# Performance work log

Hardware: AMD Instinct MI355X
Metric: run time of the kernel (lower is better)

Reference implementation:

```python
import jax, jax.numpy as jnp
import numpy as np
import math

D_MODEL = 512
N_HEADS = 8
MAX_SPAN = 512
SPAN_LOSS_COEF = 2e-4
NEG_INF = -1.0e9
R_SIZE = 4.0


def soft_span_mask(span, max_span, seq_len):
    # span: (H,) clamped span fractions
    i_idx = jnp.arange(seq_len, dtype=span.dtype)[:, None]
    j_idx = jnp.arange(seq_len, dtype=span.dtype)[None, :]
    dist = i_idx - j_idx                                  # (T, T)
    eff_span = (span * max_span)[:, None, None]           # (H, 1, 1)
    x = eff_span - dist[None, :, :]                       # (H, T, T)
    R = jnp.clip((x + 1.0) / R_SIZE, 0.0, 1.0)
    causal_ok = dist[None, :, :] >= 0
    log_R = jnp.maximum(jnp.log(R + 1e-10), NEG_INF)
    return jnp.where(causal_ok & (R > 0), log_R, NEG_INF)  # (H, T, T)


def setup_inputs() -> dict:
    key = jax.random.key(0)
    ks = jax.random.split(key, 6)
    B, T, D = 4, 2048, D_MODEL
    w_scale = 0.02
    return {
        "x": jax.random.normal(ks[0], (B, T, D), dtype=jnp.float32),
        "wq": jax.random.normal(ks[1], (D, D), dtype=jnp.float32) * w_scale,
        "wk": jax.random.normal(ks[2], (D, D), dtype=jnp.float32) * w_scale,
        "wv": jax.random.normal(ks[3], (D, D), dtype=jnp.float32) * w_scale,
        "wo": jax.random.normal(ks[4], (D, D), dtype=jnp.float32) * w_scale,
        "span_params": jax.random.uniform(ks[5], (N_HEADS,), dtype=jnp.float32),
    }


def reference(x, wq, wk, wv, wo, span_params):
    B, T, D = x.shape
    H = N_HEADS
    d_h = D // H

    clamped_span = jnp.clip(span_params, 0.0, 1.0)

    # nn.Linear(bias=False): y = x @ W.T
    Q = (x @ wq.T).reshape(B, T, H, d_h).transpose(0, 2, 1, 3)  # (B,H,T,dh)
    K = (x @ wk.T).reshape(B, T, H, d_h).transpose(0, 2, 1, 3)
    V = (x @ wv.T).reshape(B, T, H, d_h).transpose(0, 2, 1, 3)

    scale = 1.0 / math.sqrt(d_h)
    scores = jnp.einsum("bhqd,bhkd->bhqk", Q, K) * scale        # (B,H,T,T)
    scores = scores + soft_span_mask(clamped_span, MAX_SPAN, T)[None]

    weights = jax.nn.softmax(scores, axis=-1)
    out = jnp.einsum("bhqk,bhkd->bhqd", weights, V)             # (B,H,T,dh)
    out = out.transpose(0, 2, 1, 3).reshape(B, T, D)
    output = out @ wo.T

    span_loss = SPAN_LOSS_COEF * clamped_span.mean()
    return output, span_loss
```

## Files before the change

kernel.cpp:

```cpp
#include <hip/hip_runtime.h>
#include <math.h>

#define T_SEQ   2048
#define DMODEL  512
#define NHEADS  8
#define DH      64
#define NEG_INF -1.0e9f

typedef __attribute__((ext_vector_type(8))) short short8;
typedef __attribute__((ext_vector_type(4))) float f32x4;
typedef unsigned int u32;
typedef unsigned short u16;

__device__ __forceinline__ u16 f2bf(float f) {
    union { float f; u32 u; } w; w.f = f;
    return (u16)((w.u + 0x8000u) >> 16);
}

__device__ __forceinline__ void async_load16(const u16* g, u16* l) {
    __builtin_amdgcn_global_load_lds(
        (const __attribute__((address_space(1))) u32*)(const void*)g,
        (__attribute__((address_space(3))) u32*)(void*)l, 16, 0, 0);
}

__global__ void cast_all(const float* __restrict__ x,  const float* __restrict__ wq,
                         const float* __restrict__ wk, const float* __restrict__ wv,
                         const float* __restrict__ wo, const float* __restrict__ sp,
                         u16* __restrict__ xb,  u16* __restrict__ wqb,
                         u16* __restrict__ wkb, u16* __restrict__ wvb,
                         u16* __restrict__ wob, float* __restrict__ loss_out)
{
    const int bid = blockIdx.x;
    const float* src; u16* dst; int i;
    if (bid < 4096) { src = x; dst = xb; i = bid * 256 + threadIdx.x; }
    else {
        const int wsel = (bid - 4096) >> 8;
        src = (wsel == 0) ? wq : (wsel == 1) ? wk : (wsel == 2) ? wv : wo;
        dst = (wsel == 0) ? wqb : (wsel == 1) ? wkb : (wsel == 2) ? wvb : wob;
        i = ((bid - 4096) & 255) * 256 + threadIdx.x;
    }
    float4 v = ((const float4*)src)[i];
    ushort4 o;
    o.x = f2bf(v.x); o.y = f2bf(v.y); o.z = f2bf(v.z); o.w = f2bf(v.w);
    ((ushort4*)dst)[i] = o;
    if (bid == 5119 && threadIdx.x == 0) {
        float s = 0.0f;
        for (int h = 0; h < NHEADS; ++h)
            s += fminf(fmaxf(sp[h], 0.0f), 1.0f);
        loss_out[0] = 2e-4f * (s * 0.125f);
    }
}

__global__ __launch_bounds__(256)
void gemm_bf16(const u16* __restrict__ A,
               const u16* __restrict__ W0, const u16* __restrict__ W1,
               const u16* __restrict__ W2,
               u16* __restrict__ Cb0, u16* __restrict__ Cb1,
               u16* __restrict__ Cb2,
               float* __restrict__ Cf, int scatter)
{
    constexpr int K = 512, BK = 64;
    const u16* W  = (blockIdx.z == 0) ? W0 : (blockIdx.z == 1) ? W1 : W2;
    u16*       Cb = (blockIdx.z == 0) ? Cb0 : (blockIdx.z == 1) ? Cb1 : Cb2;

    __shared__ __align__(16) u16 smem[16384];
    u16* As = smem;
    u16* Bs = smem + 8192;

    const int t    = threadIdx.x;
    const int lane = t & 63;
    const int wave = t >> 6;
    const int wm   = wave >> 1, wn = wave & 1;
    const int m0   = blockIdx.x * 128, n0 = blockIdx.y * 128;

    const int srow = t >> 3;
    const int kb   = (t & 7) ^ (srow & 7);
    const u16* gA = A + (size_t)(m0 + srow) * K + kb * 8;
    const u16* gW = W + (size_t)(n0 + srow) * K + kb * 8;

    const int rA = wm * 64 + (lane & 15);
    const int rB = wn * 64 + (lane & 15);
    const int kq = lane >> 4;
    const int offA0 = rA * BK + ((kq      ^ (rA & 7)) * 8);
    const int offA1 = rA * BK + (((4 + kq) ^ (rA & 7)) * 8);
    const int offB0 = rB * BK + ((kq      ^ (rB & 7)) * 8);
    const int offB1 = rB * BK + (((4 + kq) ^ (rB & 7)) * 8);

    f32x4 acc[4][4];
#pragma unroll
    for (int it = 0; it < 4; ++it)
#pragma unroll
        for (int jt = 0; jt < 4; ++jt) acc[it][jt] = (f32x4)0.0f;

    for (int k0 = 0; k0 < K; k0 += BK) {
        __syncthreads();
#pragma unroll
        for (int i = 0; i < 4; ++i) {
            async_load16(gA + k0 + i * (32 * K), As + t * 8 + i * 2048);
            async_load16(gW + k0 + i * (32 * K), Bs + t * 8 + i * 2048);
        }
        __syncthreads();

        short8 af[4][2], bfr[4][2];
#pragma unroll
        for (int it = 0; it < 4; ++it) {
            af[it][0]  = *(const short8*)(As + offA0 + it * 16 * BK);
            af[it][1]  = *(const short8*)(As + offA1 + it * 16 * BK);
            bfr[it][0] = *(const short8*)(Bs + offB0 + it * 16 * BK);
            bfr[it][1] = *(const short8*)(Bs + offB1 + it * 16 * BK);
        }
#pragma unroll
        for (int it = 0; it < 4; ++it)
#pragma unroll
            for (int jt = 0; jt < 4; ++jt) {
                acc[it][jt] = __builtin_amdgcn_mfma_f32_16x16x32_bf16(
                    af[it][0], bfr[jt][0], acc[it][jt], 0, 0, 0);
                acc[it][jt] = __builtin_amdgcn_mfma_f32_16x16x32_bf16(
                    af[it][1], bfr[jt][1], acc[it][jt], 0, 0, 0);
            }
    }

    const int r0 = (lane >> 4) * 4;
    const int cl = lane & 15;

    if (scatter) {
        const bool vt_mode = (blockIdx.z == 2);
        constexpr int P = 136;
#pragma unroll
        for (int rnd = 0; rnd < 2; ++rnd) {
            __syncthreads();
#pragma unroll
            for (int s = 0; s < 2; ++s) {
                const int it = rnd * 2 + s;
                const int lrow = wm * 32 + s * 16 + r0;
#pragma unroll
                for (int jt = 0; jt < 4; ++jt) {
                    const int cc = wn * 64 + jt * 16 + cl;
#pragma unroll
                    for (int r = 0; r < 4; ++r)
                        smem[(lrow + r) * P + cc] = f2bf(acc[it][jt][r]);
                }
            }
            __syncthreads();
            if (!vt_mode) {
                const int lrow2 = t >> 2;
                const int h2    = (t >> 1) & 1;
                const int dhalf = t & 1;
                const int grow  = m0 + (lrow2 >> 5) * 64 + rnd * 32 + (lrow2 & 31);
                const int b     = grow >> 11, tt = grow & 2047;
                const int h     = (n0 >> 6) + h2;
                u16* dst = Cb + ((size_t)((b * NHEADS + h) * T_SEQ + tt)) * DH + dhalf * 32;
                const u16* srcl = smem + lrow2 * P + h2 * 64 + dhalf * 32;
#pragma unroll
                for (int i = 0; i < 4; ++i)
                    ((uint4*)dst)[i] = *(const uint4*)(srcl + i * 8);
            } else {
                const int hd   = t >> 1;
                const int run  = t & 1;
                const int h    = (n0 >> 6) + (hd >> 6);
                const int d    = hd & 63;
                const int tb   = m0 + run * 64 + rnd * 32;
                const int b    = tb >> 11;
                u16* dst = Cb + (((size_t)(b * NHEADS + h) * DH + d) << 11) + (tb & 2047);
                union { uint4 v[4]; u16 s[32]; } pk;
#pragma unroll
                for (int i = 0; i < 32; ++i)
                    pk.s[i] = smem[(run * 32 + i) * P + hd];
#pragma unroll
                for (int i = 0; i < 4; ++i)
                    ((uint4*)dst)[i] = pk.v[i];
            }
        }
    } else {
#pragma unroll
        for (int it = 0; it < 4; ++it) {
#pragma unroll
            for (int r = 0; r < 4; ++r) {
                const int row = m0 + wm * 64 + it * 16 + r0 + r;
#pragma unroll
                for (int jt = 0; jt < 4; ++jt) {
                    const int col = n0 + wn * 64 + jt * 16 + cl;
                    Cf[(size_t)row * DMODEL + col] = acc[it][jt][r];
                }
            }
        }
    }
}

__global__ __launch_bounds__(256)
void attn_mfma(const u16* __restrict__ Q, const u16* __restrict__ K,
               const u16* __restrict__ Vt, const float* __restrict__ span_params,
               u16* __restrict__ out)
{
    __shared__ __align__(16) u16 Ks[64 * 64];
    __shared__ __align__(16) u16 Vs[64 * 64];
    __shared__ __align__(16) u16 Ps[4][16 * 76];

    const int tid  = threadIdx.x;
    const int lane = tid & 63;
    const int w    = tid >> 6;
    const int nl   = lane & 15;
    const int quad = lane >> 4;
    const int b    = blockIdx.x & 3;
    const int h    = blockIdx.x >> 2;
    const int bh   = b * NHEADS + h;
    const int i0   = blockIdx.y * 64;
    const int q0   = i0 + w * 16;

    const u16* Qh = Q  + (size_t)bh * (T_SEQ * DH);
    const u16* Kh = K  + (size_t)bh * (T_SEQ * DH);
    const u16* Vh = Vt + (size_t)bh * (DH * T_SEQ);

    float span = span_params[h];
    span = fminf(fmaxf(span, 0.0f), 1.0f);
    const float eff_span = span * 512.0f;
    const int wspan = (int)(eff_span + 1.0f) + 1;

    short8 qf0 = *(const short8*)(Qh + (size_t)(q0 + nl) * DH + quad * 8);
    short8 qf1 = *(const short8*)(Qh + (size_t)(q0 + nl) * DH + 32 + quad * 8);

    const int srow = tid >> 2;
    const int p    = tid & 3;
    const int sw0  = ((2 * p)     ^ (srow & 7)) * 8;
    const int sw1  = ((2 * p + 1) ^ (srow & 7)) * 8;
    const u16* gK = Kh + (size_t)srow * DH + p * 16;
    const u16* gV = Vh + (size_t)srow * T_SEQ + p * 16;
    u16* lK = Ks + srow * 64;
    u16* lV = Vs + srow * 64;

    f32x4 o[4];
    float m_r[4], l_r[4];
#pragma unroll
    for (int d = 0; d < 4; ++d) o[d] = (f32x4)0.0f;
#pragma unroll
    for (int r = 0; r < 4; ++r) { m_r[r] = -1.0e30f; l_r[r] = 0.0f; }

    int j_lo = i0 - wspan;
    if (j_lo < 0) j_lo = 0;
    j_lo &= ~63;

    uint4 kr0 = *(const uint4*)(gK + (size_t)j_lo * DH);
    uint4 kr1 = *(const uint4*)(gK + (size_t)j_lo * DH + 8);
    uint4 vr0 = *(const uint4*)(gV + j_lo);
    uint4 vr1 = *(const uint4*)(gV + j_lo + 8);

    for (int j0 = j_lo; j0 <= i0; j0 += 64) {
        __syncthreads();
        *(uint4*)(lK + sw0) = kr0;
        *(uint4*)(lK + sw1) = kr1;
        *(uint4*)(lV + sw0) = vr0;
        *(uint4*)(lV + sw1) = vr1;
        __syncthreads();

        if (j0 < i0) {
            const int jn = j0 + 64;
            kr0 = *(const uint4*)(gK + (size_t)jn * DH);
            kr1 = *(const uint4*)(gK + (size_t)jn * DH + 8);
            vr0 = *(const uint4*)(gV + jn);
            vr1 = *(const uint4*)(gV + jn + 8);
        }

        f32x4 s[4];
        bool any[4];
#pragma unroll
        for (int n = 0; n < 4; ++n) {
            const int jn = j0 + n * 16;
            any[n] = (jn <= q0 + 15) &&
                     ((float)(q0 - jn - 15) < eff_span + 1.0f);
            s[n] = (f32x4)0.0f;
            if (any[n]) {
                const int row = n * 16 + nl;
                const u16* kp = Ks + row * 64;
                short8 b0 = *(const short8*)(kp + ((quad ^ (row & 7)) * 8));
                short8 b1 = *(const short8*)(kp + (((4 + quad) ^ (row & 7)) * 8));
                s[n] = __builtin_amdgcn_mfma_f32_16x16x32_bf16(qf0, b0, s[n], 0, 0, 0);
                s[n] = __builtin_amdgcn_mfma_f32_16x16x32_bf16(qf1, b1, s[n], 0, 0, 0);
            }
        }

        float tmax[4] = {-1.0e30f, -1.0e30f, -1.0e30f, -1.0e30f};
#pragma unroll
        for (int n = 0; n < 4; ++n) {
            if (!any[n]) continue;
            const int jn = j0 + n * 16;
            const bool causal_b = (jn + 15 > q0);
            const bool span_b   = ((float)(q0 + 15 - jn) > eff_span - 3.0f);
            if (!causal_b && !span_b) {
#pragma unroll
                for (int r = 0; r < 4; ++r) {
                    const float sv = s[n][r] * 0.125f;
                    s[n][r] = sv;
                    tmax[r] = fmaxf(tmax[r], sv);
                }
            } else if (!span_b) {
#pragma unroll
                for (int r = 0; r < 4; ++r) {
                    const int dist = (q0 + quad * 4 + r) - (jn + nl);
                    const float sv = (dist >= 0) ? s[n][r] * 0.125f : NEG_INF;
                    s[n][r] = sv;
                    tmax[r] = fmaxf(tmax[r], sv);
                }
            } else {
#pragma unroll
                for (int r = 0; r < 4; ++r) {
                    const int dist = (q0 + quad * 4 + r) - (jn + nl);
                    float sv = NEG_INF;
                    if (dist >= 0) {
                        float xv = eff_span - (float)dist;
                        float R  = fminf(fmaxf((xv + 1.0f) * 0.25f, 0.0f), 1.0f);
                        if (R > 0.0f)
                            sv = s[n][r] * 0.125f +
                                 ((R < 1.0f) ? __logf(R + 1e-10f) : 0.0f);
                    }
                    s[n][r] = sv;
                    tmax[r] = fmaxf(tmax[r], sv);
                }
            }
        }

        float alpha[4];
#pragma unroll
        for (int r = 0; r < 4; ++r) {
            float t = tmax[r];
            t = fmaxf(t, __shfl_xor(t, 1));
            t = fmaxf(t, __shfl_xor(t, 2));
            t = fmaxf(t, __shfl_xor(t, 4));
            t = fmaxf(t, __shfl_xor(t, 8));
            const float m_new = fmaxf(m_r[r], t);
            alpha[r] = __expf(m_r[r] - m_new);
            m_r[r] = m_new;
        }

        float psum[4] = {0.0f, 0.0f, 0.0f, 0.0f};
#pragma unroll
        for (int n = 0; n < 4; ++n) {
            if (any[n]) {
#pragma unroll
                for (int r = 0; r < 4; ++r) {
                    const float pv = __expf(s[n][r] - m_r[r]);
                    psum[r] += pv;
                    Ps[w][(quad * 4 + r) * 76 + n * 16 + nl] = f2bf(pv);
                }
            } else {
#pragma unroll
                for (int r = 0; r < 4; ++r)
                    Ps[w][(quad * 4 + r) * 76 + n * 16 + nl] = 0;
            }
        }
#pragma unroll
        for (int r = 0; r < 4; ++r) {
            float ps = psum[r];
            ps += __shfl_xor(ps, 1);
            ps += __shfl_xor(ps, 2);
            ps += __shfl_xor(ps, 4);
            ps += __shfl_xor(ps, 8);
            l_r[r] = l_r[r] * alpha[r] + ps;
#pragma unroll
            for (int d = 0; d < 4; ++d) o[d][r] *= alpha[r];
        }

        const bool kf0 = any[0] | any[1];
        const bool kf1 = any[2] | any[3];
        const u16* pb = Ps[w] + nl * 76;
        short8 a0 = *(const short8*)(pb + quad * 8);
        short8 a1 = *(const short8*)(pb + 32 + quad * 8);
#pragma unroll
        for (int d = 0; d < 4; ++d) {
            const int vrow = d * 16 + nl;
            const u16* vp = Vs + vrow * 64;
            if (kf0) {
                short8 vb0 = *(const short8*)(vp + ((quad ^ (vrow & 7)) * 8));
                o[d] = __builtin_amdgcn_mfma_f32_16x16x32_bf16(a0, vb0, o[d], 0, 0, 0);
            }
            if (kf1) {
                short8 vb1 = *(const short8*)(vp + (((4 + quad) ^ (vrow & 7)) * 8));
                o[d] = __builtin_amdgcn_mfma_f32_16x16x32_bf16(a1, vb1, o[d], 0, 0, 0);
            }
        }
    }

#pragma unroll
    for (int r = 0; r < 4; ++r) {
        const int qg = q0 + quad * 4 + r;
        const float inv_l = 1.0f / l_r[r];
        u16* op = out + (size_t)(b * T_SEQ + qg) * DMODEL + h * 64;
#pragma unroll
        for (int d = 0; d < 4; ++d)
            op[d * 16 + nl] = f2bf(o[d][r] * inv_l);
    }
}

extern "C" void kernel_launch(void* const* d_in, const int* in_sizes, int n_in,
                              void* d_out, int out_size, void* d_ws, size_t ws_size,
                              hipStream_t stream)
{
    (void)in_sizes; (void)n_in; (void)out_size; (void)ws_size;
    const float* x  = (const float*)d_in[0];
    const float* wq = (const float*)d_in[1];
    const float* wk = (const float*)d_in[2];
    const float* wv = (const float*)d_in[3];
    const float* wo = (const float*)d_in[4];
    const float* sp = (const float*)d_in[5];
    float* out = (float*)d_out;

    const size_t elems = (size_t)4 * T_SEQ * DMODEL;
    u16* xb  = (u16*)d_ws;
    u16* Qb  = xb  + elems;
    u16* Kb  = Qb  + elems;
    u16* Vtb = Kb  + elems;
    u16* Ab  = Vtb + elems;
    u16* wqb = Ab  + elems;
    u16* wkb = wqb + 262144;
    u16* wvb = wkb + 262144;
    u16* wob = wvb + 262144;

    cast_all<<<5120, 256, 0, stream>>>(x, wq, wk, wv, wo, sp,
                                       xb, wqb, wkb, wvb, wob, out + elems);
    gemm_bf16<<<dim3(64, 4, 3), 256, 0, stream>>>(
        xb, wqb, wkb, wvb, Qb, Kb, Vtb, nullptr, 1);
    attn_mfma<<<dim3(32, 32), 256, 0, stream>>>(Qb, Kb, Vtb, sp, Ab);
    gemm_bf16<<<dim3(64, 4, 1), 256, 0, stream>>>(
        Ab, wob, wob, wob, nullptr, nullptr, nullptr, out, 0);
}
```

Baseline: 171.4 us.

## Use single-wave attention blocks reading K/V from global, register-prefetch GEMM tiles

The attention kernel becomes one wave per 16-query block. It drops the shared K/V staging and block barriers, and each wave reads K and V fragments straight from global memory (relying on cache). This lets each wave iterate only over its own span window and removes synchronisation between waves, at the cost of redundant global/L2 traffic across waves that share keys. The GEMM replaces async global-to-LDS loads with register prefetch of the next K tile and sets a 3-block occupancy hint. The block-index mapping also staggers heads per batch.

```diff
diff --git a/kernel.cpp b/kernel.cpp
--- a/kernel.cpp
+++ b/kernel.cpp
@@ -15,12 +15,6 @@
 __device__ __forceinline__ u16 f2bf(float f) {
     union { float f; u32 u; } w; w.f = f;
     return (u16)((w.u + 0x8000u) >> 16);
-}
-
-__device__ __forceinline__ void async_load16(const u16* g, u16* l) {
-    __builtin_amdgcn_global_load_lds(
-        (const __attribute__((address_space(1))) u32*)(const void*)g,
-        (__attribute__((address_space(3))) u32*)(void*)l, 16, 0, 0);
 }
 
 __global__ void cast_all(const float* __restrict__ x,  const float* __restrict__ wq,
@@ -51,7 +45,7 @@
     }
 }
 
-__global__ __launch_bounds__(256)
+__global__ __launch_bounds__(256, 3)
 void gemm_bf16(const u16* __restrict__ A,
                const u16* __restrict__ W0, const u16* __restrict__ W1,
                const u16* __restrict__ W2,
@@ -92,14 +86,29 @@
 #pragma unroll
         for (int jt = 0; jt < 4; ++jt) acc[it][jt] = (f32x4)0.0f;
 
+    uint4 ar[4], wr[4];
+#pragma unroll
+    for (int i = 0; i < 4; ++i) {
+        ar[i] = *(const uint4*)(gA + i * (32 * K));
+        wr[i] = *(const uint4*)(gW + i * (32 * K));
+    }
+
     for (int k0 = 0; k0 < K; k0 += BK) {
         __syncthreads();
 #pragma unroll
         for (int i = 0; i < 4; ++i) {
-            async_load16(gA + k0 + i * (32 * K), As + t * 8 + i * 2048);
-            async_load16(gW + k0 + i * (32 * K), Bs + t * 8 + i * 2048);
+            *(uint4*)(As + t * 8 + i * 2048) = ar[i];
+            *(uint4*)(Bs + t * 8 + i * 2048) = wr[i];
         }
         __syncthreads();
+
+        if (k0 + BK < K) {
+#pragma unroll
+            for (int i = 0; i < 4; ++i) {
+                ar[i] = *(const uint4*)(gA + (k0 + BK) + i * (32 * K));
+                wr[i] = *(const uint4*)(gW + (k0 + BK) + i * (32 * K));
+            }
+        }
 
         short8 af[4][2], bfr[4][2];
 #pragma unroll
@@ -187,25 +196,21 @@
     }
 }
 
-__global__ __launch_bounds__(256)
-void attn_mfma(const u16* __restrict__ Q, const u16* __restrict__ K,
+__global__ __launch_bounds__(64, 4)
+void attn_wave(const u16* __restrict__ Q, const u16* __restrict__ K,
                const u16* __restrict__ Vt, const float* __restrict__ span_params,
                u16* __restrict__ out)
 {
-    __shared__ __align__(16) u16 Ks[64 * 64];
-    __shared__ __align__(16) u16 Vs[64 * 64];
-    __shared__ __align__(16) u16 Ps[4][16 * 76];
-
-    const int tid  = threadIdx.x;
-    const int lane = tid & 63;
-    const int w    = tid >> 6;
+    __shared__ __align__(16) u16 Ps[16 * 72];
+
+    const int lane = threadIdx.x;
     const int nl   = lane & 15;
     const int quad = lane >> 4;
-    const int b    = blockIdx.x & 3;
-    const int h    = blockIdx.x >> 2;
+    const int xi   = blockIdx.x;
+    const int b    = xi >> 3;
+    const int h    = ((xi & 7) + 5 * b) & 7;
     const int bh   = b * NHEADS + h;
-    const int i0   = blockIdx.y * 64;
-    const int q0   = i0 + w * 16;
+    const int q0   = blockIdx.y * 16;
 
     const u16* Qh = Q  + (size_t)bh * (T_SEQ * DH);
     const u16* Kh = K  + (size_t)bh * (T_SEQ * DH);
@@ -219,15 +224,6 @@
     short8 qf0 = *(const short8*)(Qh + (size_t)(q0 + nl) * DH + quad * 8);
     short8 qf1 = *(const short8*)(Qh + (size_t)(q0 + nl) * DH + 32 + quad * 8);
 
-    const int srow = tid >> 2;
-    const int p    = tid & 3;
-    const int sw0  = ((2 * p)     ^ (srow & 7)) * 8;
-    const int sw1  = ((2 * p + 1) ^ (srow & 7)) * 8;
-    const u16* gK = Kh + (size_t)srow * DH + p * 16;
-    const u16* gV = Vh + (size_t)srow * T_SEQ + p * 16;
-    u16* lK = Ks + srow * 64;
-    u16* lV = Vs + srow * 64;
-
     f32x4 o[4];
     float m_r[4], l_r[4];
 #pragma unroll
@@ -235,47 +231,41 @@
 #pragma unroll
     for (int r = 0; r < 4; ++r) { m_r[r] = -1.0e30f; l_r[r] = 0.0f; }
 
-    int j_lo = i0 - wspan;
+    int j_lo = q0 - wspan;
     if (j_lo < 0) j_lo = 0;
     j_lo &= ~63;
-
-    uint4 kr0 = *(const uint4*)(gK + (size_t)j_lo * DH);
-    uint4 kr1 = *(const uint4*)(gK + (size_t)j_lo * DH + 8);
-    uint4 vr0 = *(const uint4*)(gV + j_lo);
-    uint4 vr1 = *(const uint4*)(gV + j_lo + 8);
-
-    for (int j0 = j_lo; j0 <= i0; j0 += 64) {
-        __syncthreads();
-        *(uint4*)(lK + sw0) = kr0;
-        *(uint4*)(lK + sw1) = kr1;
-        *(uint4*)(lV + sw0) = vr0;
-        *(uint4*)(lV + sw1) = vr1;
-        __syncthreads();
-
-        if (j0 < i0) {
-            const int jn = j0 + 64;
-            kr0 = *(const uint4*)(gK + (size_t)jn * DH);
-            kr1 = *(const uint4*)(gK + (size_t)jn * DH + 8);
-            vr0 = *(const uint4*)(gV + jn);
-            vr1 = *(const uint4*)(gV + jn + 8);
-        }
-
-        f32x4 s[4];
+    const int j_hi = (q0 + 15) & ~63;
+
+    for (int j0 = j_lo; j0 <= j_hi; j0 += 64) {
         bool any[4];
 #pragma unroll
         for (int n = 0; n < 4; ++n) {
             const int jn = j0 + n * 16;
             any[n] = (jn <= q0 + 15) &&
                      ((float)(q0 - jn - 15) < eff_span + 1.0f);
+        }
+
+        f32x4 s[4];
+#pragma unroll
+        for (int n = 0; n < 4; ++n) {
             s[n] = (f32x4)0.0f;
             if (any[n]) {
-                const int row = n * 16 + nl;
-                const u16* kp = Ks + row * 64;
-                short8 b0 = *(const short8*)(kp + ((quad ^ (row & 7)) * 8));
-                short8 b1 = *(const short8*)(kp + (((4 + quad) ^ (row & 7)) * 8));
+                const u16* kp = Kh + (size_t)(j0 + n * 16 + nl) * DH + quad * 8;
+                short8 b0 = *(const short8*)kp;
+                short8 b1 = *(const short8*)(kp + 32);
                 s[n] = __builtin_amdgcn_mfma_f32_16x16x32_bf16(qf0, b0, s[n], 0, 0, 0);
                 s[n] = __builtin_amdgcn_mfma_f32_16x16x32_bf16(qf1, b1, s[n], 0, 0, 0);
             }
+        }
+
+        const bool kf0 = any[0] | any[1];
+        const bool kf1 = any[2] | any[3];
+        short8 vb0[4], vb1[4];
+#pragma unroll
+        for (int d = 0; d < 4; ++d) {
+            const u16* vp = Vh + (size_t)(d * 16 + nl) * T_SEQ + j0 + quad * 8;
+            if (kf0) vb0[d] = *(const short8*)vp;
+            if (kf1) vb1[d] = *(const short8*)(vp + 32);
         }
 
         float tmax[4] = {-1.0e30f, -1.0e30f, -1.0e30f, -1.0e30f};
@@ -339,12 +329,12 @@
                 for (int r = 0; r < 4; ++r) {
                     const float pv = __expf(s[n][r] - m_r[r]);
                     psum[r] += pv;
-                    Ps[w][(quad * 4 + r) * 76 + n * 16 + nl] = f2bf(pv);
+                    Ps[(quad * 4 + r) * 72 + n * 16 + nl] = f2bf(pv);
                 }
             } else {
 #pragma unroll
                 for (int r = 0; r < 4; ++r)
-                    Ps[w][(quad * 4 + r) * 76 + n * 16 + nl] = 0;
+                    Ps[(quad * 4 + r) * 72 + n * 16 + nl] = 0;
             }
         }
 #pragma unroll
@@ -359,23 +349,15 @@
             for (int d = 0; d < 4; ++d) o[d][r] *= alpha[r];
         }
 
-        const bool kf0 = any[0] | any[1];
-        const bool kf1 = any[2] | any[3];
-        const u16* pb = Ps[w] + nl * 76;
+        const u16* pb = Ps + nl * 72;
         short8 a0 = *(const short8*)(pb + quad * 8);
         short8 a1 = *(const short8*)(pb + 32 + quad * 8);
 #pragma unroll
         for (int d = 0; d < 4; ++d) {
-            const int vrow = d * 16 + nl;
-            const u16* vp = Vs + vrow * 64;
-            if (kf0) {
-                short8 vb0 = *(const short8*)(vp + ((quad ^ (vrow & 7)) * 8));
-                o[d] = __builtin_amdgcn_mfma_f32_16x16x32_bf16(a0, vb0, o[d], 0, 0, 0);
-            }
-            if (kf1) {
-                short8 vb1 = *(const short8*)(vp + (((4 + quad) ^ (vrow & 7)) * 8));
-                o[d] = __builtin_amdgcn_mfma_f32_16x16x32_bf16(a1, vb1, o[d], 0, 0, 0);
-            }
+            if (kf0)
+                o[d] = __builtin_amdgcn_mfma_f32_16x16x32_bf16(a0, vb0[d], o[d], 0, 0, 0);
+            if (kf1)
+                o[d] = __builtin_amdgcn_mfma_f32_16x16x32_bf16(a1, vb1[d], o[d], 0, 0, 0);
         }
     }
 
@@ -418,7 +400,7 @@
                                        xb, wqb, wkb, wvb, wob, out + elems);
     gemm_bf16<<<dim3(64, 4, 3), 256, 0, stream>>>(
         xb, wqb, wkb, wvb, Qb, Kb, Vtb, nullptr, 1);
-    attn_mfma<<<dim3(32, 32), 256, 0, stream>>>(Qb, Kb, Vtb, sp, Ab);
+    attn_wave<<<dim3(32, 128), 64, 0, stream>>>(Qb, Kb, Vtb, sp, Ab);
     gemm_bf16<<<dim3(64, 4, 1), 256, 0, stream>>>(
         Ab, wob, wob, wob, nullptr, nullptr, nullptr, out, 0);
 }
```

New measurement: 233.5 us. 1.36x slower.
